# Optimization experiments

Hardware: AMD Instinct MI355X
Metric: run time of the kernel (lower is better)

## Reference

```python
import jax, jax.numpy as jnp
import numpy as np

B = 64        # batch
N = 1024      # num_nodes
D_IN = 2      # input feature dim per node
U = 64        # num_units (hidden)
K = 2         # max_diffusion_step


def setup_inputs() -> dict:
    key = jax.random.key(0)
    ks = jax.random.split(key, 8)
    inputs = jax.random.normal(ks[0], (B, N * D_IN), dtype=jnp.float32)
    hx = jax.random.normal(ks[1], (B, N * U), dtype=jnp.float32)
    # random-walk style supports: nonnegative, row-normalized -> stable Chebyshev recursion
    a0 = jax.random.uniform(ks[2], (N, N), dtype=jnp.float32)
    a1 = jax.random.uniform(ks[3], (N, N), dtype=jnp.float32)
    support0 = a0 / jnp.sum(a0, axis=1, keepdims=True)
    support1 = a1 / jnp.sum(a1, axis=1, keepdims=True)
    num_matrices = 2 * K + 1            # len(supports)*K + 1 = 5
    in_sz = (D_IN + U) * num_matrices   # 330
    # xavier-normal init
    std_o = float(np.sqrt(2.0 / (in_sz + 2 * U)))
    std_u = float(np.sqrt(2.0 / (in_sz + U)))
    weights_output = jax.random.normal(ks[4], (in_sz, 2 * U), dtype=jnp.float32) * std_o
    weights_update = jax.random.normal(ks[5], (in_sz, U), dtype=jnp.float32) * std_u
    biases_output = jnp.ones((2 * U,), dtype=jnp.float32)
    biases_update = jnp.zeros((U,), dtype=jnp.float32)
    return {"inputs": inputs, "hx": hx, "support0": support0, "support1": support1,
            "weights_output": weights_output, "biases_output": biases_output,
            "weights_update": weights_update, "biases_update": biases_update}


def _gconv(x_cat, supports, W, b, out_size):
    # x_cat: [B, N, F]  -> Chebyshev diffusion series then dense projection
    Bsz, Nn, F = x_cat.shape
    x0 = x_cat.transpose(1, 2, 0).reshape(Nn, F * Bsz)  # [N, F*B]
    xs = [x0]
    for S in supports:
        x1 = S @ x0
        xs.append(x1)
        xk1, xk2 = x1, x0
        for _ in range(2, K + 1):
            x2 = 2.0 * (S @ xk1) - xk2
            xs.append(x2)
            xk1, xk2 = x2, xk1
    M = len(xs)                                         # num_matrices
    x = jnp.stack(xs, axis=0)                           # [M, N, F*B]
    x = x.reshape(M, Nn, F, Bsz).transpose(3, 1, 2, 0)  # [B, N, F, M]
    x = x.reshape(Bsz * Nn, F * M)
    y = x @ W + b                                       # [B*N, out_size]
    return y.reshape(Bsz, Nn * out_size)


def reference(inputs, hx, support0, support1, weights_output, biases_output,
              weights_update, biases_update):
    supports = (support0, support1)
    xi = inputs.reshape(B, N, D_IN)
    hs = hx.reshape(B, N, U)
    cat = jnp.concatenate([xi, hs], axis=2)             # [B, N, D_IN+U]
    value = jax.nn.sigmoid(_gconv(cat, supports, weights_output, biases_output, 2 * U))
    value = value.reshape(B, N, 2 * U)
    r = value[..., :U].reshape(B, N * U)
    u = value[..., U:].reshape(B, N * U)
    cat2 = jnp.concatenate([xi, (r * hx).reshape(B, N, U)], axis=2)
    c = jnp.tanh(_gconv(cat2, supports, weights_update, biases_update, U))
    return u * hx + (1.0 - u) * c
```

## Files before the change

kernel.cpp:

```cpp
#include <hip/hip_runtime.h>


typedef unsigned short u16;
typedef unsigned int u32;
typedef short s16x8 __attribute__((ext_vector_type(8)));
typedef float f32x4 __attribute__((ext_vector_type(4)));
typedef u16 u16x4 __attribute__((ext_vector_type(4)));

#define NN 1024
#define NB 64
#define NF 66
#define NCOLS 4224
#define KPAD 352
#define ASTRIDE 360

__device__ __forceinline__ u16 f2bf(float f) {
  u32 u = __builtin_bit_cast(u32, f);
  u = (u + 0x7fffu + ((u >> 16) & 1u)) >> 16;
  return (u16)u;
}
__device__ __forceinline__ float bf2f(u16 h) {
  u32 u = ((u32)h) << 16;
  return __builtin_bit_cast(float, u);
}

__device__ __forceinline__ void gload16(const void* g, void* l) {
  __builtin_amdgcn_global_load_lds(
      (const __attribute__((address_space(1))) u32*)g,
      (__attribute__((address_space(3))) u32*)l, 16, 0, 0);
}

#define CHEB_WAIT(N)                                      \
  do {                                                    \
    asm volatile("s_waitcnt vmcnt(" #N ")" ::: "memory"); \
    __builtin_amdgcn_s_barrier();                         \
    asm volatile("" ::: "memory");                        \
  } while (0)


__global__ __launch_bounds__(256) void pack_supports(
    const float* __restrict__ s0, const float* __restrict__ s1,
    u16* __restrict__ d0, u16* __restrict__ d1) {
  int i = (blockIdx.x * 256 + threadIdx.x) * 4;
  f32x4 a = *(const f32x4*)(s0 + i);
  f32x4 b = *(const f32x4*)(s1 + i);
  u16x4 oa, ob;
  oa.x = f2bf(a.x); oa.y = f2bf(a.y); oa.z = f2bf(a.z); oa.w = f2bf(a.w);
  ob.x = f2bf(b.x); ob.y = f2bf(b.y); ob.z = f2bf(b.z); ob.w = f2bf(b.w);
  *(u16x4*)(d0 + i) = oa;
  *(u16x4*)(d1 + i) = ob;
}

__global__ __launch_bounds__(64) void pack_wf(
    const float* __restrict__ W, u16* __restrict__ WF, int ldo, int nj) {
  const int c = blockIdx.x;
  const int j = blockIdx.y;
  const int lane = threadIdx.x;
  const int o = j * 16 + (lane & 15);
  const int kpb = c * 32 + (lane >> 4) * 8;
  u16 vals[8];
#pragma unroll
  for (int e = 0; e < 8; e++) {
    const int kp = kpb + e;
    float v = 0.f;
    if (kp < 330) {
      const int m = kp / 66;
      const int f = kp - m * 66;
      v = W[(f * 5 + m) * ldo + o];
    }
    vals[e] = f2bf(v);
  }
  u16* dst = WF + (((size_t)(c * nj + j) << 6) + lane) * 8;
#pragma unroll
  for (int e = 0; e < 8; e++) dst[e] = vals[e];
}

__global__ __launch_bounds__(256) void pack_x0_inputs(
    const float* __restrict__ inp, u16* __restrict__ x0t, u16* __restrict__ x0pt) {
  int b = blockIdx.x, t = threadIdx.x;
  int n4 = t * 4;
  const float* src = inp + b * 2048 + n4 * 2;
  f32x4 a = *(const f32x4*)src;
  f32x4 c = *(const f32x4*)(src + 4);
  u16x4 r0, r1;
  r0.x = f2bf(a.x); r0.y = f2bf(a.z); r0.z = f2bf(c.x); r0.w = f2bf(c.z);
  r1.x = f2bf(a.y); r1.y = f2bf(a.w); r1.z = f2bf(c.y); r1.w = f2bf(c.w);
  size_t o0 = (size_t)(b)*NN + n4;
  size_t o1 = (size_t)(64 + b) * NN + n4;
  *(u16x4*)(x0t + o0) = r0;  *(u16x4*)(x0t + o1) = r1;
  *(u16x4*)(x0pt + o0) = r0; *(u16x4*)(x0pt + o1) = r1;
}

__global__ __launch_bounds__(256) void pack_x0_hx(
    const float* __restrict__ hx, u16* __restrict__ x0t) {
  __shared__ float tile[64][65];
  int n0 = blockIdx.x * 64, b = blockIdx.y, t = threadIdx.x;
  int u4 = (t & 15) * 4, r0 = t >> 4;
#pragma unroll
  for (int p = 0; p < 4; p++) {
    int row = p * 16 + r0;
    f32x4 v = *(const f32x4*)(hx + ((size_t)b << 16) + (size_t)(n0 + row) * 64 + u4);
    tile[row][u4] = v.x; tile[row][u4 + 1] = v.y;
    tile[row][u4 + 2] = v.z; tile[row][u4 + 3] = v.w;
  }
  __syncthreads();
  int n4 = (t & 15) * 4, uu0 = t >> 4;
#pragma unroll
  for (int p = 0; p < 4; p++) {
    int u = p * 16 + uu0;
    u16x4 o;
    o.x = f2bf(tile[n4][u]);     o.y = f2bf(tile[n4 + 1][u]);
    o.z = f2bf(tile[n4 + 2][u]); o.w = f2bf(tile[n4 + 3][u]);
    *(u16x4*)&x0t[(size_t)((2 + u) * 64 + b) * NN + n0 + n4] = o;
  }
}


__global__ __launch_bounds__(256, 3) void cheb_gemm(
    const u16* __restrict__ S0, const u16* __restrict__ S1,
    const u16* __restrict__ Xi0, const u16* __restrict__ Xi1,
    u16* __restrict__ Xo0, u16* __restrict__ Xo1,
    const u16* __restrict__ Xprev, int use_prev) {
  __shared__ u16 As[3][128 * 32];
  __shared__ u16 Bs[3][128 * 32];
  const int t = threadIdx.x;
  const int lane = t & 63;
  const int w = t >> 6;

  const int lid = blockIdx.x;
  const int work = (lid & 7) * 66 + (lid >> 3);
  const int y = work & 7;
  const int tt = work >> 3;
  const int x = tt % 33;
  const int z = tt / 33;
  const int n0 = x * 128;
  const int m0 = y * 128;
  const u16* S = z ? S1 : S0;
  const u16* Xi = z ? Xi1 : Xi0;
  u16* Xo = z ? Xo1 : Xo0;

  const int swz = ((lane & 3) ^ ((lane >> 3) & 3)) * 8;
  const int rl = lane >> 2;
  const u16* pA0 = S + (size_t)(m0 + w * 32 + rl) * NN + swz;
  const u16* pA1 = pA0 + (size_t)16 * NN;
  const u16* pB0 = Xi + (size_t)(n0 + w * 32 + rl) * NN + swz;
  const u16* pB1 = pB0 + (size_t)16 * NN;
  const int db0 = (w * 32) * 32;
  const int db1 = (w * 32 + 16) * 32;

  const int wm = (w >> 1) * 64;
  const int wn = (w & 1) * 64;
  const int fr = lane & 15;
  const int q = lane >> 4;
  const int fo = (q ^ ((fr >> 1) & 3)) * 8;

  f32x4 acc[4][4];
#pragma unroll
  for (int i = 0; i < 4; i++)
#pragma unroll
    for (int j = 0; j < 4; j++) acc[i][j] = f32x4{0.f, 0.f, 0.f, 0.f};

  auto stage = [&](u16* dA, u16* dB) {
    gload16(pA0, dA + db0);
    gload16(pA1, dA + db1);
    gload16(pB0, dB + db0);
    gload16(pB1, dB + db1);
    pA0 += 32; pA1 += 32; pB0 += 32; pB1 += 32;
  };
  auto compute = [&](const u16* cA, const u16* cB) {
    s16x8 af[4], bfr[4];
#pragma unroll
    for (int i = 0; i < 4; i++)
      af[i] = *(const s16x8*)&cA[(wm + i * 16 + fr) * 32 + fo];
#pragma unroll
    for (int j = 0; j < 4; j++)
      bfr[j] = *(const s16x8*)&cB[(wn + j * 16 + fr) * 32 + fo];
#pragma unroll
    for (int i = 0; i < 4; i++)
#pragma unroll
      for (int j = 0; j < 4; j++)
        acc[i][j] = __builtin_amdgcn_mfma_f32_16x16x32_bf16(af[i], bfr[j], acc[i][j], 0, 0, 0);
  };

  u16* a0 = &As[0][0]; u16* a1 = &As[1][0]; u16* a2 = &As[2][0];
  u16* b0 = &Bs[0][0]; u16* b1 = &Bs[1][0]; u16* b2 = &Bs[2][0];

  stage(a0, b0);
  stage(a1, b1);
#pragma unroll 1
  for (int it = 0; it < 10; it++) {
    CHEB_WAIT(4); stage(a2, b2); compute(a0, b0);
    CHEB_WAIT(4); stage(a0, b0); compute(a1, b1);
    CHEB_WAIT(4); stage(a1, b1); compute(a2, b2);
  }
  CHEB_WAIT(4); compute(a0, b0);
  CHEB_WAIT(0); compute(a1, b1);

  const int nr0 = (lane >> 4) << 2;
#pragma unroll
  for (int i = 0; i < 4; i++) {
    const int node = m0 + wm + i * 16 + nr0;
#pragma unroll
    for (int j = 0; j < 4; j++) {
      const int colg = n0 + wn + j * 16 + fr;
      size_t off = (size_t)colg * NN + node;
      f32x4 c = acc[i][j];
      if (use_prev) {
        u16x4 p = *(const u16x4*)&Xprev[off];
        c.x = 2.f * c.x - bf2f(p.x);
        c.y = 2.f * c.y - bf2f(p.y);
        c.z = 2.f * c.z - bf2f(p.z);
        c.w = 2.f * c.w - bf2f(p.w);
      }
      u16x4 o;
      o.x = f2bf(c.x); o.y = f2bf(c.y); o.z = f2bf(c.z); o.w = f2bf(c.w);
      *(u16x4*)&Xo[off] = o;
    }
  }
}


__device__ __forceinline__ void proj_stage(
    u16* A, const u16* __restrict__ X0, const u16* __restrict__ X1,
    const u16* __restrict__ X2, const u16* __restrict__ X3,
    const u16* __restrict__ X4, int b, int n0, int t) {
  for (int idx = t; idx < 1408; idx += 256) {
    const int kp0 = (idx >> 4) * 4;
    const int n4 = (idx & 15) * 4;
    u16x4 v[4];
#pragma unroll
    for (int r = 0; r < 4; r++) {
      const int kp = kp0 + r;
      if (kp < 330) {
        const int m = kp / 66;
        const int f = kp - m * 66;
        const u16* Xm = m == 0 ? X0 : m == 1 ? X1 : m == 2 ? X2 : m == 3 ? X3 : X4;
        v[r] = *(const u16x4*)(Xm + (size_t)(f * 64 + b) * NN + n0 + n4);
      } else {
        v[r] = u16x4{0, 0, 0, 0};
      }
    }
#pragma unroll
    for (int c = 0; c < 4; c++) {
      u16x4 o;
      o.x = v[0][c]; o.y = v[1][c]; o.z = v[2][c]; o.w = v[3][c];
      *(u16x4*)&A[(n4 + c) * ASTRIDE + kp0] = o;
    }
  }
}

__global__ __launch_bounds__(256) void proj1(
    const u16* __restrict__ X0, const u16* __restrict__ X1, const u16* __restrict__ X2,
    const u16* __restrict__ X3, const u16* __restrict__ X4,
    const u16* __restrict__ WF, const float* __restrict__ bias,
    const float* __restrict__ hx, u16* __restrict__ X0p, float* __restrict__ uout) {
  __shared__ u16 A[64 * ASTRIDE];
  const int t = threadIdx.x;
  const int n0 = blockIdx.x * 64;
  const int b = blockIdx.y;
  proj_stage(A, X0, X1, X2, X3, X4, b, n0, t);
  __syncthreads();

  const int lane = t & 63;
  const int w = t >> 6;
  const int fr = lane & 15;
  const int q8 = (lane >> 4) * 8;
  const u16* arow = &A[(w * 16 + fr) * ASTRIDE + q8];
  const u16* wfl = WF + (size_t)lane * 8;

  f32x4 acc[8];
#pragma unroll
  for (int j = 0; j < 8; j++) acc[j] = f32x4{0.f, 0.f, 0.f, 0.f};

  for (int c = 0; c < 11; c++) {
    const s16x8 af = *(const s16x8*)(arow + c * 32);
#pragma unroll
    for (int j = 0; j < 8; j++) {
      const s16x8 bf = *(const s16x8*)(wfl + ((c * 8 + j) << 9));
      acc[j] = __builtin_amdgcn_mfma_f32_16x16x32_bf16(af, bf, acc[j], 0, 0, 0);
    }
  }

  const int nl0 = (lane >> 4) * 4;
  const int n = n0 + w * 16 + nl0;
#pragma unroll
  for (int j = 0; j < 8; j++) {
    const int o = j * 16 + fr;
    const float bs = bias[o];
    f32x4 v;
    v.x = 1.f / (1.f + __expf(-(acc[j].x + bs)));
    v.y = 1.f / (1.f + __expf(-(acc[j].y + bs)));
    v.z = 1.f / (1.f + __expf(-(acc[j].z + bs)));
    v.w = 1.f / (1.f + __expf(-(acc[j].w + bs)));
    if (o < 64) {
      const float* hxp = hx + ((size_t)b << 16) + (size_t)n * 64 + o;
      u16x4 s;
      s.x = f2bf(v.x * hxp[0 * 64]);
      s.y = f2bf(v.y * hxp[1 * 64]);
      s.z = f2bf(v.z * hxp[2 * 64]);
      s.w = f2bf(v.w * hxp[3 * 64]);
      *(u16x4*)&X0p[(size_t)((2 + o) * 64 + b) * NN + n] = s;
    } else {
      float* up = uout + (((size_t)b << 10) + n) * 64 + (o - 64);
      up[0 * 64] = v.x; up[1 * 64] = v.y; up[2 * 64] = v.z; up[3 * 64] = v.w;
    }
  }
}

__global__ __launch_bounds__(256) void proj2(
    const u16* __restrict__ X0, const u16* __restrict__ X1, const u16* __restrict__ X2,
    const u16* __restrict__ X3, const u16* __restrict__ X4,
    const u16* __restrict__ WF, const float* __restrict__ bias,
    const float* __restrict__ hx, const float* uin, float* out) {
  __shared__ u16 A[64 * ASTRIDE];
  const int t = threadIdx.x;
  const int n0 = blockIdx.x * 64;
  const int b = blockIdx.y;
  proj_stage(A, X0, X1, X2, X3, X4, b, n0, t);
  __syncthreads();

  const int lane = t & 63;
  const int w = t >> 6;
  const int fr = lane & 15;
  const int q8 = (lane >> 4) * 8;
  const u16* arow = &A[(w * 16 + fr) * ASTRIDE + q8];
  const u16* wfl = WF + (size_t)lane * 8;

  f32x4 acc[4];
#pragma unroll
  for (int j = 0; j < 4; j++) acc[j] = f32x4{0.f, 0.f, 0.f, 0.f};

  for (int c = 0; c < 11; c++) {
    const s16x8 af = *(const s16x8*)(arow + c * 32);
#pragma unroll
    for (int j = 0; j < 4; j++) {
      const s16x8 bf = *(const s16x8*)(wfl + ((c * 4 + j) << 9));
      acc[j] = __builtin_amdgcn_mfma_f32_16x16x32_bf16(af, bf, acc[j], 0, 0, 0);
    }
  }

  const int nl0 = (lane >> 4) * 4;
  const int n = n0 + w * 16 + nl0;
#pragma unroll
  for (int j = 0; j < 4; j++) {
    const int o = j * 16 + fr;
    const float bs = bias[o];
    const size_t base = (((size_t)b << 10) + n) * 64 + o;
    float c0 = tanhf(acc[j].x + bs);
    float c1 = tanhf(acc[j].y + bs);
    float c2 = tanhf(acc[j].z + bs);
    float c3 = tanhf(acc[j].w + bs);
    float u0 = uin[base + 0 * 64], u1 = uin[base + 1 * 64];
    float u2 = uin[base + 2 * 64], u3 = uin[base + 3 * 64];
    float h0 = hx[base + 0 * 64], h1 = hx[base + 1 * 64];
    float h2 = hx[base + 2 * 64], h3 = hx[base + 3 * 64];
    out[base + 0 * 64] = u0 * h0 + (1.f - u0) * c0;
    out[base + 1 * 64] = u1 * h1 + (1.f - u1) * c1;
    out[base + 2 * 64] = u2 * h2 + (1.f - u2) * c2;
    out[base + 3 * 64] = u3 * h3 + (1.f - u3) * c3;
  }
}


extern "C" void kernel_launch(void* const* d_in, const int* in_sizes, int n_in,
                              void* d_out, int out_size, void* d_ws, size_t ws_size,
                              hipStream_t stream) {
  (void)in_sizes; (void)n_in; (void)out_size; (void)ws_size;
  const float* inp = (const float*)d_in[0];
  const float* hx  = (const float*)d_in[1];
  const float* s0  = (const float*)d_in[2];
  const float* s1  = (const float*)d_in[3];
  const float* Wo  = (const float*)d_in[4];
  const float* bo  = (const float*)d_in[5];
  const float* Wu  = (const float*)d_in[6];
  const float* bu  = (const float*)d_in[7];
  float* out = (float*)d_out;

  char* p = (char*)d_ws;
  u16* Sb0 = (u16*)p; p += (size_t)NN * NN * 2;
  u16* Sb1 = (u16*)p; p += (size_t)NN * NN * 2;
  const size_t xbytes = (size_t)NCOLS * NN * 2;
  u16* X0T = (u16*)p; p += xbytes;
  u16* X1T = (u16*)p; p += xbytes;
  u16* X2T = (u16*)p; p += xbytes;
  u16* X3T = (u16*)p; p += xbytes;
  u16* X4T = (u16*)p; p += xbytes;
  u16* X0P = (u16*)p; p += xbytes;
  u16* WF1 = (u16*)p; p += (size_t)11 * 8 * 512 * 2;
  u16* WF2 = (u16*)p; p += (size_t)11 * 4 * 512 * 2;

  pack_supports<<<dim3(1024), dim3(256), 0, stream>>>(s0, s1, Sb0, Sb1);
  pack_wf<<<dim3(11, 8), dim3(64), 0, stream>>>(Wo, WF1, 128, 8);
  pack_wf<<<dim3(11, 4), dim3(64), 0, stream>>>(Wu, WF2, 64, 4);
  pack_x0_inputs<<<dim3(64), dim3(256), 0, stream>>>(inp, X0T, X0P);
  pack_x0_hx<<<dim3(16, 64), dim3(256), 0, stream>>>(hx, X0T);
  cheb_gemm<<<dim3(528), dim3(256), 0, stream>>>(Sb0, Sb1, X0T, X0T, X1T, X3T,
                                                 (const u16*)nullptr, 0);
  cheb_gemm<<<dim3(528), dim3(256), 0, stream>>>(Sb0, Sb1, X1T, X3T, X2T, X4T, X0T, 1);
  proj1<<<dim3(16, 64), dim3(256), 0, stream>>>(X0T, X1T, X2T, X3T, X4T, WF1, bo, hx, X0P, out);
  cheb_gemm<<<dim3(528), dim3(256), 0, stream>>>(Sb0, Sb1, X0P, X0P, X1T, X3T,
                                                 (const u16*)nullptr, 0);
  cheb_gemm<<<dim3(528), dim3(256), 0, stream>>>(Sb0, Sb1, X1T, X3T, X2T, X4T, X0P, 1);
  proj2<<<dim3(16, 64), dim3(256), 0, stream>>>(X0P, X1T, X2T, X3T, X4T, WF2, bu, hx, out, out);
}
```

Before: 289.1 us.

## Fold Chebyshev 2x-minus-prev into projection weights; merge pack kernels

```diff
diff --git a/kernel.cpp b/kernel.cpp
--- a/kernel.cpp
+++ b/kernel.cpp
@@ -52,9 +52,13 @@
 }
 
 __global__ __launch_bounds__(64) void pack_wf(
-    const float* __restrict__ W, u16* __restrict__ WF, int ldo, int nj) {
+    const float* __restrict__ Wo, const float* __restrict__ Wu,
+    u16* __restrict__ WF1, u16* __restrict__ WF2) {
   const int c = blockIdx.x;
-  const int j = blockIdx.y;
+  int j = blockIdx.y;
+  const float* W; u16* WF; int ldo, nj;
+  if (j < 8) { W = Wo; WF = WF1; ldo = 128; nj = 8; }
+  else       { j -= 8; W = Wu; WF = WF2; ldo = 64; nj = 4; }
   const int lane = threadIdx.x;
   const int o = j * 16 + (lane & 15);
   const int kpb = c * 32 + (lane >> 4) * 8;
@@ -66,7 +70,11 @@
     if (kp < 330) {
       const int m = kp / 66;
       const int f = kp - m * 66;
-      v = W[(f * 5 + m) * ldo + o];
+      const float* Wrow = W + (size_t)(f * 5) * ldo + o;
+      if (m == 0)      v = Wrow[0] - Wrow[2 * ldo] - Wrow[4 * ldo];
+      else if (m == 2) v = 2.f * Wrow[2 * ldo];
+      else if (m == 4) v = 2.f * Wrow[4 * ldo];
+      else             v = Wrow[(size_t)m * ldo];
     }
     vals[e] = f2bf(v);
   }
@@ -75,26 +83,21 @@
   for (int e = 0; e < 8; e++) dst[e] = vals[e];
 }
 
-__global__ __launch_bounds__(256) void pack_x0_inputs(
-    const float* __restrict__ inp, u16* __restrict__ x0t, u16* __restrict__ x0pt) {
-  int b = blockIdx.x, t = threadIdx.x;
-  int n4 = t * 4;
-  const float* src = inp + b * 2048 + n4 * 2;
-  f32x4 a = *(const f32x4*)src;
-  f32x4 c = *(const f32x4*)(src + 4);
-  u16x4 r0, r1;
-  r0.x = f2bf(a.x); r0.y = f2bf(a.z); r0.z = f2bf(c.x); r0.w = f2bf(c.z);
-  r1.x = f2bf(a.y); r1.y = f2bf(a.w); r1.z = f2bf(c.y); r1.w = f2bf(c.w);
-  size_t o0 = (size_t)(b)*NN + n4;
-  size_t o1 = (size_t)(64 + b) * NN + n4;
-  *(u16x4*)(x0t + o0) = r0;  *(u16x4*)(x0t + o1) = r1;
-  *(u16x4*)(x0pt + o0) = r0; *(u16x4*)(x0pt + o1) = r1;
-}
-
-__global__ __launch_bounds__(256) void pack_x0_hx(
-    const float* __restrict__ hx, u16* __restrict__ x0t) {
+__global__ __launch_bounds__(256) void pack_x0(
+    const float* __restrict__ inp, const float* __restrict__ hx,
+    u16* __restrict__ x0t, u16* __restrict__ x0pt) {
   __shared__ float tile[64][65];
   int n0 = blockIdx.x * 64, b = blockIdx.y, t = threadIdx.x;
+  if (t < 32) {
+    const int f = t >> 4;
+    const int n4 = (t & 15) * 4;
+    const float* src = inp + b * 2048 + (n0 + n4) * 2 + f;
+    u16x4 o;
+    o.x = f2bf(src[0]); o.y = f2bf(src[2]); o.z = f2bf(src[4]); o.w = f2bf(src[6]);
+    size_t off = (size_t)(f * 64 + b) * NN + n0 + n4;
+    *(u16x4*)(x0t + off) = o;
+    *(u16x4*)(x0pt + off) = o;
+  }
   int u4 = (t & 15) * 4, r0 = t >> 4;
 #pragma unroll
   for (int p = 0; p < 4; p++) {
@@ -119,8 +122,7 @@
 __global__ __launch_bounds__(256, 3) void cheb_gemm(
     const u16* __restrict__ S0, const u16* __restrict__ S1,
     const u16* __restrict__ Xi0, const u16* __restrict__ Xi1,
-    u16* __restrict__ Xo0, u16* __restrict__ Xo1,
-    const u16* __restrict__ Xprev, int use_prev) {
+    u16* __restrict__ Xo0, u16* __restrict__ Xo1) {
   __shared__ u16 As[3][128 * 32];
   __shared__ u16 Bs[3][128 * 32];
   const int t = threadIdx.x;
@@ -205,13 +207,6 @@
       const int colg = n0 + wn + j * 16 + fr;
       size_t off = (size_t)colg * NN + node;
       f32x4 c = acc[i][j];
-      if (use_prev) {
-        u16x4 p = *(const u16x4*)&Xprev[off];
-        c.x = 2.f * c.x - bf2f(p.x);
-        c.y = 2.f * c.y - bf2f(p.y);
-        c.z = 2.f * c.z - bf2f(p.z);
-        c.w = 2.f * c.w - bf2f(p.w);
-      }
       u16x4 o;
       o.x = f2bf(c.x); o.y = f2bf(c.y); o.z = f2bf(c.z); o.w = f2bf(c.w);
       *(u16x4*)&Xo[off] = o;
@@ -390,16 +385,12 @@
   u16* WF2 = (u16*)p; p += (size_t)11 * 4 * 512 * 2;
 
   pack_supports<<<dim3(1024), dim3(256), 0, stream>>>(s0, s1, Sb0, Sb1);
-  pack_wf<<<dim3(11, 8), dim3(64), 0, stream>>>(Wo, WF1, 128, 8);
-  pack_wf<<<dim3(11, 4), dim3(64), 0, stream>>>(Wu, WF2, 64, 4);
-  pack_x0_inputs<<<dim3(64), dim3(256), 0, stream>>>(inp, X0T, X0P);
-  pack_x0_hx<<<dim3(16, 64), dim3(256), 0, stream>>>(hx, X0T);
-  cheb_gemm<<<dim3(528), dim3(256), 0, stream>>>(Sb0, Sb1, X0T, X0T, X1T, X3T,
-                                                 (const u16*)nullptr, 0);
-  cheb_gemm<<<dim3(528), dim3(256), 0, stream>>>(Sb0, Sb1, X1T, X3T, X2T, X4T, X0T, 1);
+  pack_wf<<<dim3(11, 12), dim3(64), 0, stream>>>(Wo, Wu, WF1, WF2);
+  pack_x0<<<dim3(16, 64), dim3(256), 0, stream>>>(inp, hx, X0T, X0P);
+  cheb_gemm<<<dim3(528), dim3(256), 0, stream>>>(Sb0, Sb1, X0T, X0T, X1T, X3T);
+  cheb_gemm<<<dim3(528), dim3(256), 0, stream>>>(Sb0, Sb1, X1T, X3T, X2T, X4T);
   proj1<<<dim3(16, 64), dim3(256), 0, stream>>>(X0T, X1T, X2T, X3T, X4T, WF1, bo, hx, X0P, out);
-  cheb_gemm<<<dim3(528), dim3(256), 0, stream>>>(Sb0, Sb1, X0P, X0P, X1T, X3T,
-                                                 (const u16*)nullptr, 0);
-  cheb_gemm<<<dim3(528), dim3(256), 0, stream>>>(Sb0, Sb1, X1T, X3T, X2T, X4T, X0P, 1);
+  cheb_gemm<<<dim3(528), dim3(256), 0, stream>>>(Sb0, Sb1, X0P, X0P, X1T, X3T);
+  cheb_gemm<<<dim3(528), dim3(256), 0, stream>>>(Sb0, Sb1, X1T, X3T, X2T, X4T);
   proj2<<<dim3(16, 64), dim3(256), 0, stream>>>(X0P, X1T, X2T, X3T, X4T, WF2, bu, hx, out, out);
 }
```

Result: faster. 274.5 us (-5.1%).
